# Kernel tuning notes

Measured on AMD Instinct MI355X. Metric: run time of the kernel, lower is better.

Reference implementation:

```python
import jax, jax.numpy as jnp
import numpy as np

B, M, N = 16384, 512, 2048
N_ITERS = 10


def setup_inputs() -> dict:
    key = jax.random.key(0)
    kb, kD = jax.random.split(key)
    batch = jax.random.normal(kb, (B, M), dtype=jnp.float32)
    # nn.Parameter(torch.rand((M, N))) -> uniform [0,1)
    D = jax.random.uniform(kD, (M, N), dtype=jnp.float32)
    gamma = jnp.float32(0.1)
    beta = jnp.float32(0.1)
    return {"batch": batch, "D": D, "gamma": gamma, "beta": beta}


def reference(batch, D, gamma, beta):
    # Vectorized AMP sparse coding: the original loops over batch items; here
    # the per-sample matvecs D.T@v and D@alpha become batched GEMMs v@D, a@D.T.
    y = batch                                   # [B, M]
    m = D.shape[0]
    sqrt_m = jnp.sqrt(jnp.asarray(m, y.dtype))
    alpha0 = jnp.zeros((y.shape[0], D.shape[1]), dtype=y.dtype)  # [B, N]

    def amp_step(carry, _):
        alpha, v = carry
        z = alpha + beta * (v @ D)                               # [B, N]
        # per-sample threshold t = gamma/sqrt(M) * ||v||_2
        t = (gamma / sqrt_m) * jnp.linalg.norm(v, axis=-1, keepdims=True)  # [B,1]
        new_alpha = jnp.maximum(z - t, 0.0) * jnp.sign(z)        # relu(z-t)*sign(z)
        new_v = (y - beta * (new_alpha @ D.T)
                 + (beta / m) * jnp.linalg.norm(new_alpha, axis=-1, keepdims=True) * v)
        return (new_alpha, new_v), None

    (alpha, _v), _ = jax.lax.scan(amp_step, (alpha0, y), None, length=N_ITERS)
    return alpha
```

## Files before the change

kernel.cpp:

```cpp
#include <hip/hip_runtime.h>
#include <math.h>

#define Bsz 16384
#define Msz 512
#define Nsz 2048

typedef _Float16 half8 __attribute__((ext_vector_type(8)));
typedef _Float16 half4 __attribute__((ext_vector_type(4)));
typedef _Float16 half2v __attribute__((ext_vector_type(2)));
typedef float floatx16 __attribute__((ext_vector_type(16)));
typedef unsigned int uint;

struct HL { _Float16 h, l; };
__device__ __forceinline__ HL split1(float x) {
    HL r;
    r.h = (_Float16)x;
    r.l = (_Float16)(x - (float)r.h);
    return r;
}
__device__ __forceinline__ uint packHL(float x) {
    HL s = split1(x);
    return (uint)__builtin_bit_cast(unsigned short, s.h)
         | ((uint)__builtin_bit_cast(unsigned short, s.l) << 16);
}
__device__ __forceinline__ float unpackHL(uint w) {
    half2v p = __builtin_bit_cast(half2v, w);
    return (float)p.x + (float)p.y;
}

__device__ __forceinline__ void gl_lds16(const _Float16* g, _Float16* l) {
    __builtin_amdgcn_global_load_lds(
        (const __attribute__((address_space(1))) unsigned int*)g,
        (__attribute__((address_space(3))) unsigned int*)l, 16, 0, 0);
}

#define BAR()  asm volatile("s_barrier" ::: "memory")


__global__ __launch_bounds__(256) void zero_kernel(float4* __restrict__ p) {
    p[blockIdx.x * 256 + threadIdx.x] = make_float4(0.f, 0.f, 0.f, 0.f);
}

__global__ __launch_bounds__(256) void init_kernel(const float* __restrict__ batch,
        _Float16* __restrict__ vh, float* __restrict__ t2) {
    const int wave = threadIdx.x >> 6;
    const int lane = threadIdx.x & 63;
    const int b = (blockIdx.x << 2) + wave;
    const float* row = batch + (size_t)b * Msz + lane * 8;
    float4 a = *(const float4*)row;
    float4 c = *(const float4*)(row + 4);
    half8 h;
    h[0] = (_Float16)a.x; h[1] = (_Float16)a.y;
    h[2] = (_Float16)a.z; h[3] = (_Float16)a.w;
    h[4] = (_Float16)c.x; h[5] = (_Float16)c.y;
    h[6] = (_Float16)c.z; h[7] = (_Float16)c.w;
    const size_t off = ((size_t)(b >> 5) * 32 + (lane >> 1)) * 512
                     + ((size_t)(lane & 1) << 8) + ((b & 31) << 3);
    *(half8*)(vh + off) = h;
    float s = a.x*a.x + a.y*a.y + a.z*a.z + a.w*a.w
            + c.x*c.x + c.y*c.y + c.z*c.z + c.w*c.w;
#pragma unroll
    for (int off2 = 32; off2 > 0; off2 >>= 1) s += __shfl_down(s, off2);
    if (lane == 0) t2[b] = s;
}

__global__ __launch_bounds__(256) void convD_kernel(const float* __restrict__ D,
        _Float16* __restrict__ Dph, _Float16* __restrict__ Dtph) {
    __shared__ float T[64][65];
    const int t = threadIdx.x;
    const int tx = t & 15, ty = t >> 4;
    const int n0 = blockIdx.x << 6, m0 = blockIdx.y << 6;
#pragma unroll
    for (int q = 0; q < 4; ++q) {
        const int mr = m0 + (ty << 2) + q;
        const int nc = n0 + (tx << 2);
        float4 d = *(const float4*)(D + (size_t)mr * Nsz + nc);
        half4 h;
        h[0] = (_Float16)d.x; h[1] = (_Float16)d.y;
        h[2] = (_Float16)d.z; h[3] = (_Float16)d.w;
        const size_t o2 = ((size_t)(mr >> 5) * 128 + (nc >> 4)) * 512
                        + (((size_t)(nc >> 3) & 1) << 8) + ((mr & 31) << 3) + (nc & 7);
        *(half4*)(Dph + o2) = h;
        T[(tx << 2) + 0][(ty << 2) + q] = d.x;
        T[(tx << 2) + 1][(ty << 2) + q] = d.y;
        T[(tx << 2) + 2][(ty << 2) + q] = d.z;
        T[(tx << 2) + 3][(ty << 2) + q] = d.w;
    }
    __syncthreads();
#pragma unroll
    for (int q = 0; q < 4; ++q) {
        const int nr = n0 + (ty << 2) + q;
        const int mc = m0 + (tx << 2);
        float4 d = make_float4(T[(ty << 2) + q][tx << 2],
                               T[(ty << 2) + q][(tx << 2) + 1],
                               T[(ty << 2) + q][(tx << 2) + 2],
                               T[(ty << 2) + q][(tx << 2) + 3]);
        half4 h;
        h[0] = (_Float16)d.x; h[1] = (_Float16)d.y;
        h[2] = (_Float16)d.z; h[3] = (_Float16)d.w;
        const size_t o1 = ((size_t)(nr >> 5) * 32 + (mc >> 4)) * 512
                        + (((size_t)(mc >> 3) & 1) << 8) + ((nr & 31) << 3) + (mc & 7);
        *(half4*)(Dtph + o1) = h;
    }
}

__global__ __launch_bounds__(512, 4) void gemm1_kernel(
        const _Float16* __restrict__ Av,
        const _Float16* __restrict__ Bth,
        const float* __restrict__ t2,
        uint* __restrict__ alphaP,
        float* __restrict__ na2,
        const float* __restrict__ beta_p, const float* __restrict__ gamma_p,
        int first, int last) {
    __shared__ _Float16 lds[24576];

    const int tid = threadIdx.x;
    const int wave = tid >> 6, lane = tid & 63;
    const int wy = wave >> 1, wx = wave & 1;
    const int ln = lane & 31, lh = lane >> 5;
    const int bid = blockIdx.x;
    const int b0 = (bid & 63) << 8;
    const int n0 = (bid >> 6) << 7;
    const int R0 = b0 >> 5, C0 = n0 >> 5;

    floatx16 acc[2][2] = {};

    const _Float16* pb[6];
#pragma unroll
    for (int e = 0; e < 6; ++e) {
        const int f = wave * 6 + e;
        const bool isB = f >= 32;
        const int q = isB ? f - 32 : f;
        const int t = q >> 2, kt = q & 3;
        const _Float16* base = isB ? Bth : Av;
        const int T0 = isB ? C0 : R0;
        pb[e] = base + ((size_t)(T0 + t) * 32) * 512 + (size_t)kt * 512 + lane * 8;
    }
    const int f0 = wave * 6;

    const int ro = lane << 3;

    for (int c = 0; c < 8; ++c) {
        __syncthreads();
#pragma unroll
        for (int e = 0; e < 6; ++e)
            gl_lds16(pb[e] + (size_t)c * 2048, lds + ((f0 + e) << 9));
        __builtin_amdgcn_s_waitcnt(0);
        __syncthreads();

#pragma unroll
        for (int ks = 0; ks < 4; ++ks) {
            half8 fa[2], fb[2];
#pragma unroll
            for (int i = 0; i < 2; ++i) {
                fa[i] = *(const half8*)(lds + ((((wy * 2 + i) << 2) + ks) << 9) + ro);
                fb[i] = *(const half8*)(lds + 16384 + ((((wx * 2 + i) << 2) + ks) << 9) + ro);
            }
#pragma unroll
            for (int j = 0; j < 2; ++j)
#pragma unroll
                for (int i = 0; i < 2; ++i)
                    acc[i][j] = __builtin_amdgcn_mfma_f32_32x32x16_f16(fa[i], fb[j], acc[i][j], 0, 0, 0);
        }
    }

    const float beta = beta_p[0];
    const float tc = gamma_p[0] * 0.044194173824159216f;
#pragma unroll
    for (int i = 0; i < 2; ++i) {
#pragma unroll
        for (int reg = 0; reg < 16; ++reg) {
            const int rr = (reg & 3) + 8 * (reg >> 2) + 4 * lh;
            const int b = b0 + wy * 64 + i * 32 + rr;
            const float tb2 = tc * sqrtf(t2[b]);
            uint* arow = alphaP + (size_t)b * Nsz + n0 + wx * 64 + ln;
            float s = 0.f;
#pragma unroll
            for (int j = 0; j < 2; ++j) {
                float z = first ? 0.f : unpackHL(arow[j * 32]);
                float val = fmaxf(fmaf(beta, acc[i][j][reg], z) - tb2, 0.f);
                if (last) ((float*)arow)[j * 32] = val;
                else      arow[j * 32] = packHL(val);
                s = fmaf(val, val, s);
            }
            s += __shfl_down(s, 16, 32);
            s += __shfl_down(s, 8, 32);
            s += __shfl_down(s, 4, 32);
            s += __shfl_down(s, 2, 32);
            s += __shfl_down(s, 1, 32);
            if (ln == 0) atomicAdd(&na2[b], s);
        }
    }
}

__global__ __launch_bounds__(512, 2) void gemm2_kernel(
        const uint* __restrict__ alphaP,
        const _Float16* __restrict__ Bh,
        const float* __restrict__ na2,
        const float* __restrict__ y,
        _Float16* __restrict__ vh,
        float* __restrict__ t2,
        const float* __restrict__ beta_p) {
    __shared__ _Float16 lds[24576];

    const int tid = threadIdx.x;
    const int wave = tid >> 6, lane = tid & 63;
    const int wy = wave >> 1, wx = wave & 1;
    const int ln = lane & 31, lh = lane >> 5;
    const int bid = blockIdx.x;
    const int b0 = (bid & 63) << 8;
    const int m0 = (bid >> 6) << 7;
    const int C0 = m0 >> 5;

    floatx16 acc[2][2] = {};

    const int srow = tid >> 1;
    const int skq  = (tid & 1) << 4;
    const uint* apP = alphaP + (size_t)(b0 + srow) * Nsz + skq;
    const int awo = ((((srow >> 5) << 1) + (skq >> 4)) << 9) + ((srow & 31) << 3);

    const _Float16* gB = Bh + ((size_t)(C0 + (wave >> 1)) * 128) * 512
                       + (size_t)(wave & 1) * 512 + lane * 8;
    const int fB = 16 + wave;

    const int ro = lane << 3;

    uint4 a0, a1, a2, a3;
    auto loadA = [&](int c) {
        const uint* nx = apP + c * 32;
        a0 = *(const uint4*)(nx);
        a1 = *(const uint4*)(nx + 4);
        a2 = *(const uint4*)(nx + 8);
        a3 = *(const uint4*)(nx + 12);
    };
    auto writeA = [&](int d) {
        uint4 ha, hb;
        ha.x = __builtin_amdgcn_perm(a0.y, a0.x, 0x05040100u);
        ha.y = __builtin_amdgcn_perm(a0.w, a0.z, 0x05040100u);
        ha.z = __builtin_amdgcn_perm(a1.y, a1.x, 0x05040100u);
        ha.w = __builtin_amdgcn_perm(a1.w, a1.z, 0x05040100u);
        hb.x = __builtin_amdgcn_perm(a2.y, a2.x, 0x05040100u);
        hb.y = __builtin_amdgcn_perm(a2.w, a2.z, 0x05040100u);
        hb.z = __builtin_amdgcn_perm(a3.y, a3.x, 0x05040100u);
        hb.w = __builtin_amdgcn_perm(a3.w, a3.z, 0x05040100u);
        _Float16* aw = lds + d * 12288 + awo;
        *(uint4*)aw = ha;
        *(uint4*)(aw + 256) = hb;
    };
    auto stageB = [&](int c, int d) {
        gl_lds16(gB + (size_t)c * 1024, lds + d * 12288 + (fB << 9));
    };

    loadA(0);
    writeA(0);
    stageB(0, 0);
    loadA(1);
    writeA(1);
    stageB(1, 1);
    loadA(2);
    asm volatile("s_waitcnt vmcnt(5) lgkmcnt(0)" ::: "memory");
    BAR();

    for (int c = 0; c < 64; ++c) {
        const _Float16* lb = lds + (c & 1) * 12288;
        __builtin_amdgcn_s_setprio(1);
#pragma unroll
        for (int ks = 0; ks < 2; ++ks) {
            half8 fa[2], fb[2];
#pragma unroll
            for (int i = 0; i < 2; ++i) {
                fa[i] = *(const half8*)(lb + ((((wy * 2 + i) << 1) + ks) << 9) + ro);
                fb[i] = *(const half8*)(lb + 8192 + ((((wx * 2 + i) << 1) + ks) << 9) + ro);
            }
#pragma unroll
            for (int j = 0; j < 2; ++j)
#pragma unroll
                for (int i = 0; i < 2; ++i)
                    acc[i][j] = __builtin_amdgcn_mfma_f32_32x32x16_f16(fa[i], fb[j], acc[i][j], 0, 0, 0);
        }
        __builtin_amdgcn_s_setprio(0);
        if (c == 63) break;
        BAR();
        if (c < 62) {
            stageB(c + 2, c & 1);
            writeA(c & 1);
            if (c < 61) loadA(c + 3);
            asm volatile("s_waitcnt vmcnt(5) lgkmcnt(0)" ::: "memory");
        } else {
            asm volatile("s_waitcnt vmcnt(0) lgkmcnt(0)" ::: "memory");
        }
        BAR();
    }

    const float beta = beta_p[0];
#pragma unroll
    for (int i = 0; i < 2; ++i) {
#pragma unroll
        for (int reg = 0; reg < 16; ++reg) {
            const int rr = (reg & 3) + 8 * (reg >> 2) + 4 * lh;
            const int b = b0 + wy * 64 + i * 32 + rr;
            const float cb = beta * (1.0f / 512.0f) * sqrtf(na2[b]);
            float s = 0.f;
#pragma unroll
            for (int j = 0; j < 2; ++j) {
                const int m = m0 + wx * 64 + j * 32 + ln;
                const size_t po = ((size_t)(b >> 5) * 32 + (m >> 4)) * 512
                                + (((size_t)(m >> 3) & 1) << 8) + ((b & 31) << 3) + (m & 7);
                const size_t yi = (size_t)b * Msz + m;
                float vold = (float)vh[po];
                float val = y[yi] - beta * acc[i][j][reg] + cb * vold;
                vh[po] = (_Float16)val;
                s = fmaf(val, val, s);
            }
            s += __shfl_down(s, 16, 32);
            s += __shfl_down(s, 8, 32);
            s += __shfl_down(s, 4, 32);
            s += __shfl_down(s, 2, 32);
            s += __shfl_down(s, 1, 32);
            if (ln == 0) atomicAdd(&t2[b], s);
        }
    }
}

extern "C" void kernel_launch(void* const* d_in, const int* in_sizes, int n_in,
                              void* d_out, int out_size, void* d_ws, size_t ws_size,
                              hipStream_t stream) {
    (void)in_sizes; (void)n_in; (void)out_size; (void)ws_size;
    const float* batch   = (const float*)d_in[0];
    const float* D       = (const float*)d_in[1];
    const float* gamma_p = (const float*)d_in[2];
    const float* beta_p  = (const float*)d_in[3];

    uint* alphaP = (uint*)d_out;

    _Float16* vh   = (_Float16*)d_ws;
    _Float16* Dph  = vh + (size_t)Bsz * Msz;
    _Float16* Dtph = Dph + (size_t)Msz * Nsz;
    float*    t2s  = (float*)(Dtph + (size_t)Msz * Nsz);
    float*    na2s = t2s + 10 * Bsz;

    zero_kernel<<<19 * Bsz / 1024, 256, 0, stream>>>((float4*)(t2s + Bsz));
    convD_kernel<<<dim3(Nsz / 64, Msz / 64), 256, 0, stream>>>(D, Dph, Dtph);
    init_kernel<<<Bsz / 4, 256, 0, stream>>>(batch, vh, t2s);

    for (int it = 0; it < 10; ++it) {
        gemm1_kernel<<<1024, 512, 0, stream>>>(vh, Dtph,
                                               t2s + (size_t)it * Bsz,
                                               alphaP,
                                               na2s + (size_t)it * Bsz,
                                               beta_p, gamma_p,
                                               it == 0 ? 1 : 0, it == 9 ? 1 : 0);
        if (it < 9) {
            gemm2_kernel<<<256, 512, 0, stream>>>(alphaP, Dph,
                                                  na2s + (size_t)it * Bsz,
                                                  batch, vh,
                                                  t2s + (size_t)(it + 1) * Bsz,
                                                  beta_p);
        }
    }
}
```

Measured before the change: 1.785 ms.

## Fuse all AMP iterations into one persistent kernel per 32-row batch tile

Replaces the per-iteration pair of GEMM kernels with a single kernel in which each 1024-thread block owns 32 batch rows for all ten iterations. Alpha stays in MFMA accumulator registers and v stays in LDS, which removes the global round-trips for alpha, v and the norm buffers as well as the repeated launches. The hi/lo split encoding of alpha is dropped and beta is folded into v and the threshold. The trade-off is that D and D^T fragments are now streamed from global memory (L2) by every block each iteration with no LDS staging or pipelining, and the 32-row M tile gives low reuse of D.

```diff
diff --git a/kernel.cpp b/kernel.cpp
--- a/kernel.cpp
+++ b/kernel.cpp
@@ -7,62 +7,9 @@
 
 typedef _Float16 half8 __attribute__((ext_vector_type(8)));
 typedef _Float16 half4 __attribute__((ext_vector_type(4)));
-typedef _Float16 half2v __attribute__((ext_vector_type(2)));
 typedef float floatx16 __attribute__((ext_vector_type(16)));
 typedef unsigned int uint;
 
-struct HL { _Float16 h, l; };
-__device__ __forceinline__ HL split1(float x) {
-    HL r;
-    r.h = (_Float16)x;
-    r.l = (_Float16)(x - (float)r.h);
-    return r;
-}
-__device__ __forceinline__ uint packHL(float x) {
-    HL s = split1(x);
-    return (uint)__builtin_bit_cast(unsigned short, s.h)
-         | ((uint)__builtin_bit_cast(unsigned short, s.l) << 16);
-}
-__device__ __forceinline__ float unpackHL(uint w) {
-    half2v p = __builtin_bit_cast(half2v, w);
-    return (float)p.x + (float)p.y;
-}
-
-__device__ __forceinline__ void gl_lds16(const _Float16* g, _Float16* l) {
-    __builtin_amdgcn_global_load_lds(
-        (const __attribute__((address_space(1))) unsigned int*)g,
-        (__attribute__((address_space(3))) unsigned int*)l, 16, 0, 0);
-}
-
-#define BAR()  asm volatile("s_barrier" ::: "memory")
-
-
-__global__ __launch_bounds__(256) void zero_kernel(float4* __restrict__ p) {
-    p[blockIdx.x * 256 + threadIdx.x] = make_float4(0.f, 0.f, 0.f, 0.f);
-}
-
-__global__ __launch_bounds__(256) void init_kernel(const float* __restrict__ batch,
-        _Float16* __restrict__ vh, float* __restrict__ t2) {
-    const int wave = threadIdx.x >> 6;
-    const int lane = threadIdx.x & 63;
-    const int b = (blockIdx.x << 2) + wave;
-    const float* row = batch + (size_t)b * Msz + lane * 8;
-    float4 a = *(const float4*)row;
-    float4 c = *(const float4*)(row + 4);
-    half8 h;
-    h[0] = (_Float16)a.x; h[1] = (_Float16)a.y;
-    h[2] = (_Float16)a.z; h[3] = (_Float16)a.w;
-    h[4] = (_Float16)c.x; h[5] = (_Float16)c.y;
-    h[6] = (_Float16)c.z; h[7] = (_Float16)c.w;
-    const size_t off = ((size_t)(b >> 5) * 32 + (lane >> 1)) * 512
-                     + ((size_t)(lane & 1) << 8) + ((b & 31) << 3);
-    *(half8*)(vh + off) = h;
-    float s = a.x*a.x + a.y*a.y + a.z*a.z + a.w*a.w
-            + c.x*c.x + c.y*c.y + c.z*c.z + c.w*c.w;
-#pragma unroll
-    for (int off2 = 32; off2 > 0; off2 >>= 1) s += __shfl_down(s, off2);
-    if (lane == 0) t2[b] = s;
-}
 
 __global__ __launch_bounds__(256) void convD_kernel(const float* __restrict__ D,
         _Float16* __restrict__ Dph, _Float16* __restrict__ Dtph) {
@@ -104,222 +51,173 @@
     }
 }
 
-__global__ __launch_bounds__(512, 4) void gemm1_kernel(
-        const _Float16* __restrict__ Av,
-        const _Float16* __restrict__ Bth,
-        const float* __restrict__ t2,
-        uint* __restrict__ alphaP,
-        float* __restrict__ na2,
-        const float* __restrict__ beta_p, const float* __restrict__ gamma_p,
-        int first, int last) {
-    __shared__ _Float16 lds[24576];
+__global__ __launch_bounds__(1024, 4) void amp_kernel(
+        const float* __restrict__ y,
+        const _Float16* __restrict__ Dt,
+        const _Float16* __restrict__ Dp,
+        const float* __restrict__ beta_p,
+        const float* __restrict__ gamma_p,
+        float* __restrict__ out) {
+    __shared__ _Float16 alpha_lds[32768];
+    __shared__ _Float16 v_lds[16384];
+    __shared__ float t2s[32];
+    __shared__ float na2[32];
 
     const int tid = threadIdx.x;
-    const int wave = tid >> 6, lane = tid & 63;
-    const int wy = wave >> 1, wx = wave & 1;
+    const int w = tid >> 6;
+    const int lane = tid & 63;
     const int ln = lane & 31, lh = lane >> 5;
-    const int bid = blockIdx.x;
-    const int b0 = (bid & 63) << 8;
-    const int n0 = (bid >> 6) << 7;
-    const int R0 = b0 >> 5, C0 = n0 >> 5;
-
-    floatx16 acc[2][2] = {};
-
-    const _Float16* pb[6];
-#pragma unroll
-    for (int e = 0; e < 6; ++e) {
-        const int f = wave * 6 + e;
-        const bool isB = f >= 32;
-        const int q = isB ? f - 32 : f;
-        const int t = q >> 2, kt = q & 3;
-        const _Float16* base = isB ? Bth : Av;
-        const int T0 = isB ? C0 : R0;
-        pb[e] = base + ((size_t)(T0 + t) * 32) * 512 + (size_t)kt * 512 + lane * 8;
-    }
-    const int f0 = wave * 6;
-
-    const int ro = lane << 3;
-
-    for (int c = 0; c < 8; ++c) {
-        __syncthreads();
-#pragma unroll
-        for (int e = 0; e < 6; ++e)
-            gl_lds16(pb[e] + (size_t)c * 2048, lds + ((f0 + e) << 9));
-        __builtin_amdgcn_s_waitcnt(0);
-        __syncthreads();
-
-#pragma unroll
-        for (int ks = 0; ks < 4; ++ks) {
-            half8 fa[2], fb[2];
-#pragma unroll
-            for (int i = 0; i < 2; ++i) {
-                fa[i] = *(const half8*)(lds + ((((wy * 2 + i) << 2) + ks) << 9) + ro);
-                fb[i] = *(const half8*)(lds + 16384 + ((((wx * 2 + i) << 2) + ks) << 9) + ro);
-            }
-#pragma unroll
-            for (int j = 0; j < 2; ++j)
-#pragma unroll
-                for (int i = 0; i < 2; ++i)
-                    acc[i][j] = __builtin_amdgcn_mfma_f32_32x32x16_f16(fa[i], fb[j], acc[i][j], 0, 0, 0);
-        }
-    }
+    const int b0 = blockIdx.x << 5;
 
     const float beta = beta_p[0];
-    const float tc = gamma_p[0] * 0.044194173824159216f;
-#pragma unroll
-    for (int i = 0; i < 2; ++i) {
+    const float tcoef = gamma_p[0] * 0.044194173824159216f / beta;
+
+    if (tid < 32) na2[tid] = 0.f;
+    {
+        const int b = tid >> 5, mg = tid & 31;
+        const float* yr = y + (size_t)(b0 + b) * Msz + mg * 16;
+        float s = 0.f;
+#pragma unroll
+        for (int u4 = 0; u4 < 4; ++u4) {
+            float4 f = *(const float4*)(yr + u4 * 4);
+            float vals[4] = {f.x, f.y, f.z, f.w};
+#pragma unroll
+            for (int e = 0; e < 4; ++e) {
+                float bv = beta * vals[e];
+                s = fmaf(bv, bv, s);
+                const int m = mg * 16 + u4 * 4 + e;
+                v_lds[(m >> 4) * 512 + ((m >> 3) & 1) * 256 + b * 8 + (m & 7)] =
+                    (_Float16)bv;
+            }
+        }
+#pragma unroll
+        for (int off = 16; off > 0; off >>= 1) s += __shfl_down(s, off, 32);
+        if (mg == 0) t2s[b] = s;
+    }
+    __syncthreads();
+
+    floatx16 z[4] = {};
+
+    for (int it = 0; it < 10; ++it) {
+        for (int kt = 0; kt < 32; ++kt) {
+            half8 A = *(const half8*)(v_lds + kt * 512 + lane * 8);
+            half8 Bf[4];
+#pragma unroll
+            for (int s = 0; s < 4; ++s)
+                Bf[s] = *(const half8*)(Dt + (((size_t)(4 * w + s) * 32 + kt) << 9)
+                                        + lane * 8);
+#pragma unroll
+            for (int s = 0; s < 4; ++s)
+                z[s] = __builtin_amdgcn_mfma_f32_32x32x16_f16(A, Bf[s], z[s], 0, 0, 0);
+        }
+
 #pragma unroll
         for (int reg = 0; reg < 16; ++reg) {
             const int rr = (reg & 3) + 8 * (reg >> 2) + 4 * lh;
-            const int b = b0 + wy * 64 + i * 32 + rr;
-            const float tb2 = tc * sqrtf(t2[b]);
-            uint* arow = alphaP + (size_t)b * Nsz + n0 + wx * 64 + ln;
-            float s = 0.f;
-#pragma unroll
-            for (int j = 0; j < 2; ++j) {
-                float z = first ? 0.f : unpackHL(arow[j * 32]);
-                float val = fmaxf(fmaf(beta, acc[i][j][reg], z) - tb2, 0.f);
-                if (last) ((float*)arow)[j * 32] = val;
-                else      arow[j * 32] = packHL(val);
-                s = fmaf(val, val, s);
-            }
-            s += __shfl_down(s, 16, 32);
-            s += __shfl_down(s, 8, 32);
-            s += __shfl_down(s, 4, 32);
-            s += __shfl_down(s, 2, 32);
-            s += __shfl_down(s, 1, 32);
-            if (ln == 0) atomicAdd(&na2[b], s);
-        }
-    }
-}
-
-__global__ __launch_bounds__(512, 2) void gemm2_kernel(
-        const uint* __restrict__ alphaP,
-        const _Float16* __restrict__ Bh,
-        const float* __restrict__ na2,
-        const float* __restrict__ y,
-        _Float16* __restrict__ vh,
-        float* __restrict__ t2,
-        const float* __restrict__ beta_p) {
-    __shared__ _Float16 lds[24576];
-
-    const int tid = threadIdx.x;
-    const int wave = tid >> 6, lane = tid & 63;
-    const int wy = wave >> 1, wx = wave & 1;
-    const int ln = lane & 31, lh = lane >> 5;
-    const int bid = blockIdx.x;
-    const int b0 = (bid & 63) << 8;
-    const int m0 = (bid >> 6) << 7;
-    const int C0 = m0 >> 5;
-
-    floatx16 acc[2][2] = {};
-
-    const int srow = tid >> 1;
-    const int skq  = (tid & 1) << 4;
-    const uint* apP = alphaP + (size_t)(b0 + srow) * Nsz + skq;
-    const int awo = ((((srow >> 5) << 1) + (skq >> 4)) << 9) + ((srow & 31) << 3);
-
-    const _Float16* gB = Bh + ((size_t)(C0 + (wave >> 1)) * 128) * 512
-                       + (size_t)(wave & 1) * 512 + lane * 8;
-    const int fB = 16 + wave;
-
-    const int ro = lane << 3;
-
-    uint4 a0, a1, a2, a3;
-    auto loadA = [&](int c) {
-        const uint* nx = apP + c * 32;
-        a0 = *(const uint4*)(nx);
-        a1 = *(const uint4*)(nx + 4);
-        a2 = *(const uint4*)(nx + 8);
-        a3 = *(const uint4*)(nx + 12);
-    };
-    auto writeA = [&](int d) {
-        uint4 ha, hb;
-        ha.x = __builtin_amdgcn_perm(a0.y, a0.x, 0x05040100u);
-        ha.y = __builtin_amdgcn_perm(a0.w, a0.z, 0x05040100u);
-        ha.z = __builtin_amdgcn_perm(a1.y, a1.x, 0x05040100u);
-        ha.w = __builtin_amdgcn_perm(a1.w, a1.z, 0x05040100u);
-        hb.x = __builtin_amdgcn_perm(a2.y, a2.x, 0x05040100u);
-        hb.y = __builtin_amdgcn_perm(a2.w, a2.z, 0x05040100u);
-        hb.z = __builtin_amdgcn_perm(a3.y, a3.x, 0x05040100u);
-        hb.w = __builtin_amdgcn_perm(a3.w, a3.z, 0x05040100u);
-        _Float16* aw = lds + d * 12288 + awo;
-        *(uint4*)aw = ha;
-        *(uint4*)(aw + 256) = hb;
-    };
-    auto stageB = [&](int c, int d) {
-        gl_lds16(gB + (size_t)c * 1024, lds + d * 12288 + (fB << 9));
-    };
-
-    loadA(0);
-    writeA(0);
-    stageB(0, 0);
-    loadA(1);
-    writeA(1);
-    stageB(1, 1);
-    loadA(2);
-    asm volatile("s_waitcnt vmcnt(5) lgkmcnt(0)" ::: "memory");
-    BAR();
-
-    for (int c = 0; c < 64; ++c) {
-        const _Float16* lb = lds + (c & 1) * 12288;
-        __builtin_amdgcn_s_setprio(1);
-#pragma unroll
-        for (int ks = 0; ks < 2; ++ks) {
-            half8 fa[2], fb[2];
-#pragma unroll
-            for (int i = 0; i < 2; ++i) {
-                fa[i] = *(const half8*)(lb + ((((wy * 2 + i) << 1) + ks) << 9) + ro);
-                fb[i] = *(const half8*)(lb + 8192 + ((((wx * 2 + i) << 1) + ks) << 9) + ro);
-            }
-#pragma unroll
-            for (int j = 0; j < 2; ++j)
-#pragma unroll
-                for (int i = 0; i < 2; ++i)
-                    acc[i][j] = __builtin_amdgcn_mfma_f32_32x32x16_f16(fa[i], fb[j], acc[i][j], 0, 0, 0);
-        }
-        __builtin_amdgcn_s_setprio(0);
-        if (c == 63) break;
-        BAR();
-        if (c < 62) {
-            stageB(c + 2, c & 1);
-            writeA(c & 1);
-            if (c < 61) loadA(c + 3);
-            asm volatile("s_waitcnt vmcnt(5) lgkmcnt(0)" ::: "memory");
-        } else {
-            asm volatile("s_waitcnt vmcnt(0) lgkmcnt(0)" ::: "memory");
-        }
-        BAR();
-    }
-
-    const float beta = beta_p[0];
-#pragma unroll
-    for (int i = 0; i < 2; ++i) {
+            const float tb = tcoef * sqrtf(t2s[rr]);
+            float ns = 0.f;
+#pragma unroll
+            for (int s = 0; s < 4; ++s) {
+                float val = fmaxf(z[s][reg] - tb, 0.f);
+                z[s][reg] = val;
+                ns = fmaf(val, val, ns);
+            }
+            if (it < 9) {
+                ns += __shfl_down(ns, 16, 32);
+                ns += __shfl_down(ns, 8, 32);
+                ns += __shfl_down(ns, 4, 32);
+                ns += __shfl_down(ns, 2, 32);
+                ns += __shfl_down(ns, 1, 32);
+                if (ln == 0) atomicAdd(&na2[rr], ns);
+            }
+        }
+
+        if (it == 9) break;
+
+        __syncthreads();
+        if (tid < 32) t2s[tid] = 0.f;
+
+        floatx16 a2;
+        {
+            const int m = (w << 5) + ln;
+            const float* yc = y + (size_t)b0 * Msz + m;
+#pragma unroll
+            for (int reg = 0; reg < 16; ++reg) {
+                const int rr = (reg & 3) + 8 * (reg >> 2) + 4 * lh;
+                const float cb = sqrtf(na2[rr]) * (1.0f / 512.0f);
+                const float vold = (float)v_lds[(m >> 4) * 512 + ((m >> 3) & 1) * 256
+                                                + rr * 8 + (m & 7)];
+                a2[reg] = yc[(size_t)rr * Msz] + cb * vold;
+            }
+        }
+
+        if (w < 8) {
+#pragma unroll
+            for (int s = 0; s < 4; ++s)
+#pragma unroll
+                for (int reg = 0; reg < 16; ++reg) {
+                    const int rr = (reg & 3) + 8 * (reg >> 2) + 4 * lh;
+                    const int n = (w << 7) + (s << 5) + ln;
+                    alpha_lds[(n >> 4) * 512 + ((n >> 3) & 1) * 256 + rr * 8 + (n & 7)]
+                        = (_Float16)(-beta * z[s][reg]);
+                }
+        }
+        __syncthreads();
+        if (tid < 32) na2[tid] = 0.f;
+
+        for (int kt = 0; kt < 64; ++kt) {
+            half8 A = *(const half8*)(alpha_lds + kt * 512 + lane * 8);
+            half8 Bf = *(const half8*)(Dp + (((size_t)w * 128 + kt) << 9) + lane * 8);
+            a2 = __builtin_amdgcn_mfma_f32_32x32x16_f16(A, Bf, a2, 0, 0, 0);
+        }
+        __syncthreads();
+
+        if (w >= 8) {
+#pragma unroll
+            for (int s = 0; s < 4; ++s)
+#pragma unroll
+                for (int reg = 0; reg < 16; ++reg) {
+                    const int rr = (reg & 3) + 8 * (reg >> 2) + 4 * lh;
+                    const int n = (w << 7) + (s << 5) + ln;
+                    alpha_lds[((n >> 4) - 64) * 512 + ((n >> 3) & 1) * 256
+                              + rr * 8 + (n & 7)]
+                        = (_Float16)(-beta * z[s][reg]);
+                }
+        }
+        __syncthreads();
+        for (int kt = 64; kt < 128; ++kt) {
+            half8 A = *(const half8*)(alpha_lds + (kt - 64) * 512 + lane * 8);
+            half8 Bf = *(const half8*)(Dp + (((size_t)w * 128 + kt) << 9) + lane * 8);
+            a2 = __builtin_amdgcn_mfma_f32_32x32x16_f16(A, Bf, a2, 0, 0, 0);
+        }
+
+        {
+            const int m = (w << 5) + ln;
+#pragma unroll
+            for (int reg = 0; reg < 16; ++reg) {
+                const int rr = (reg & 3) + 8 * (reg >> 2) + 4 * lh;
+                const float bv = beta * a2[reg];
+                v_lds[(m >> 4) * 512 + ((m >> 3) & 1) * 256 + rr * 8 + (m & 7)] =
+                    (_Float16)bv;
+                float ts = bv * bv;
+                ts += __shfl_down(ts, 16, 32);
+                ts += __shfl_down(ts, 8, 32);
+                ts += __shfl_down(ts, 4, 32);
+                ts += __shfl_down(ts, 2, 32);
+                ts += __shfl_down(ts, 1, 32);
+                if (ln == 0) atomicAdd(&t2s[rr], ts);
+            }
+        }
+        __syncthreads();
+    }
+
+#pragma unroll
+    for (int s = 0; s < 4; ++s)
 #pragma unroll
         for (int reg = 0; reg < 16; ++reg) {
             const int rr = (reg & 3) + 8 * (reg >> 2) + 4 * lh;
-            const int b = b0 + wy * 64 + i * 32 + rr;
-            const float cb = beta * (1.0f / 512.0f) * sqrtf(na2[b]);
-            float s = 0.f;
-#pragma unroll
-            for (int j = 0; j < 2; ++j) {
-                const int m = m0 + wx * 64 + j * 32 + ln;
-                const size_t po = ((size_t)(b >> 5) * 32 + (m >> 4)) * 512
-                                + (((size_t)(m >> 3) & 1) << 8) + ((b & 31) << 3) + (m & 7);
-                const size_t yi = (size_t)b * Msz + m;
-                float vold = (float)vh[po];
-                float val = y[yi] - beta * acc[i][j][reg] + cb * vold;
-                vh[po] = (_Float16)val;
-                s = fmaf(val, val, s);
-            }
-            s += __shfl_down(s, 16, 32);
-            s += __shfl_down(s, 8, 32);
-            s += __shfl_down(s, 4, 32);
-            s += __shfl_down(s, 2, 32);
-            s += __shfl_down(s, 1, 32);
-            if (ln == 0) atomicAdd(&t2[b], s);
-        }
-    }
+            out[(size_t)(b0 + rr) * Nsz + (w << 7) + (s << 5) + ln] = z[s][reg];
+        }
 }
 
 extern "C" void kernel_launch(void* const* d_in, const int* in_sizes, int n_in,
@@ -331,31 +229,10 @@
     const float* gamma_p = (const float*)d_in[2];
     const float* beta_p  = (const float*)d_in[3];
 
-    uint* alphaP = (uint*)d_out;
-
-    _Float16* vh   = (_Float16*)d_ws;
-    _Float16* Dph  = vh + (size_t)Bsz * Msz;
+    _Float16* Dph  = (_Float16*)d_ws;
     _Float16* Dtph = Dph + (size_t)Msz * Nsz;
-    float*    t2s  = (float*)(Dtph + (size_t)Msz * Nsz);
-    float*    na2s = t2s + 10 * Bsz;
-
-    zero_kernel<<<19 * Bsz / 1024, 256, 0, stream>>>((float4*)(t2s + Bsz));
+
     convD_kernel<<<dim3(Nsz / 64, Msz / 64), 256, 0, stream>>>(D, Dph, Dtph);
-    init_kernel<<<Bsz / 4, 256, 0, stream>>>(batch, vh, t2s);
-
-    for (int it = 0; it < 10; ++it) {
-        gemm1_kernel<<<1024, 512, 0, stream>>>(vh, Dtph,
-                                               t2s + (size_t)it * Bsz,
-                                               alphaP,
-                                               na2s + (size_t)it * Bsz,
-                                               beta_p, gamma_p,
-                                               it == 0 ? 1 : 0, it == 9 ? 1 : 0);
-        if (it < 9) {
-            gemm2_kernel<<<256, 512, 0, stream>>>(alphaP, Dph,
-                                                  na2s + (size_t)it * Bsz,
-                                                  batch, vh,
-                                                  t2s + (size_t)(it + 1) * Bsz,
-                                                  beta_p);
-        }
-    }
+    amp_kernel<<<Bsz / 32, 1024, 0, stream>>>(batch, Dtph, Dph,
+                                              beta_p, gamma_p, (float*)d_out);
 }
```

After: 5.331 ms. +198.6%, slower.
